# Kernel tuning notes

Hardware: AMD Instinct MI355X
Metric: run time of the kernel (lower is better)

## Reference

```python
import jax, jax.numpy as jnp
import numpy as np

EPS = 1e-5

def _ln(x, w, b):
    mu = jnp.mean(x, -1, keepdims=True)
    var = jnp.mean((x - mu) ** 2, -1, keepdims=True)
    return (x - mu) * jax.lax.rsqrt(var + EPS) * w + b

def setup_inputs() -> dict:
    key = jax.random.key(0)
    ks = jax.random.split(key, 12)
    B, H, W, C = 4, 32, 32, 768
    nh, hd, hidden = 12, 64, 3072
    s = lambda k, sh, fan: jax.random.normal(k, sh, jnp.float32) * (fan ** -0.5)
    return {
        "x": jax.random.normal(ks[0], (B, H, W, C), jnp.float32),
        "norm1_w": jnp.ones((C,), jnp.float32),
        "norm1_b": jnp.zeros((C,), jnp.float32),
        "qkv_w": s(ks[1], (C, 3 * C), C),
        "qkv_b": jnp.zeros((3 * C,), jnp.float32),
        "proj_w": s(ks[2], (C, C), C),
        "proj_b": jnp.zeros((C,), jnp.float32),
        "rel_h": jnp.ones((2 * H - 1, hd), jnp.float32),
        "rel_w": jnp.ones((2 * W - 1, hd), jnp.float32),
        "norm2_w": jnp.ones((C,), jnp.float32),
        "norm2_b": jnp.zeros((C,), jnp.float32),
        "mlp_w1": s(ks[3], (C, hidden), C),
        "mlp_b1": jnp.zeros((hidden,), jnp.float32),
        "mlp_w2": s(ks[4], (hidden, C), hidden),
        "mlp_b2": jnp.zeros((C,), jnp.float32),
    }

def reference(x, norm1_w, norm1_b, qkv_w, qkv_b, proj_w, proj_b, rel_h, rel_w,
              norm2_w, norm2_b, mlp_w1, mlp_b1, mlp_w2, mlp_b2):
    B, H, W, C = x.shape
    nh = 12
    hd = C // nh
    scale = hd ** -0.5
    S = H * W

    xn = _ln(x, norm1_w, norm1_b)
    qkv = (xn.reshape(B, S, C) @ qkv_w + qkv_b)            # [B,S,3C]
    qkv = qkv.reshape(B, S, 3, nh, hd).transpose(2, 0, 3, 1, 4).reshape(3, B * nh, S, hd)
    q, k, v = qkv[0], qkv[1], qkv[2]                        # [B*nh,S,hd]

    attn = jnp.einsum('bqd,bkd->bqk', q * scale, k)         # [B*nh,S,S]

    # relative position bias (q_size == k_size == H or W)
    idx_h = jnp.arange(H)[:, None] - jnp.arange(H)[None, :] + (H - 1)
    idx_w = jnp.arange(W)[:, None] - jnp.arange(W)[None, :] + (W - 1)
    Rh = rel_h[idx_h]                                       # [H,H,hd]
    Rw = rel_w[idx_w]                                       # [W,W,hd]
    q4 = q.reshape(B * nh, H, W, hd)                        # unscaled q, as in source
    bias_h = jnp.einsum('bhwc,hkc->bhwk', q4, Rh)           # [B*nh,H,W,H]
    bias_w = jnp.einsum('bhwc,wkc->bhwk', q4, Rw)           # [B*nh,H,W,W]
    attn = (attn.reshape(B * nh, H, W, H, W)
            + bias_h[:, :, :, :, None]
            + bias_w[:, :, :, None, :]).reshape(B * nh, S, S)

    attn = jax.nn.softmax(attn, axis=-1)
    out = jnp.einsum('bqk,bkd->bqd', attn, v)               # [B*nh,S,hd]
    out = out.reshape(B, nh, H, W, hd).transpose(0, 2, 3, 1, 4).reshape(B, H, W, C)
    x = out @ proj_w + proj_b + x

    xn = _ln(x, norm2_w, norm2_b)
    h = jax.nn.gelu(xn @ mlp_w1 + mlp_b1, approximate=False)
    return h @ mlp_w2 + mlp_b2 + x
```

## Files before the change

kernel.cpp:

```cpp
#include <hip/hip_runtime.h>
#include <hip/hip_bf16.h>
#include <cstdint>
#include <cstddef>

typedef __bf16 bf16x8 __attribute__((ext_vector_type(8)));
typedef float  f32x4  __attribute__((ext_vector_type(4)));
typedef unsigned short u16x8 __attribute__((ext_vector_type(8)));

#define S_TOT 1024
#define NH 12
#define HD 64
#define NBH 48
#define CDIM 768
#define L2E 1.44269504088896f

static __device__ __forceinline__ unsigned short f2bf(float f) {
    unsigned int u = __builtin_bit_cast(unsigned int, f);
    u += 0x7FFFu + ((u >> 16) & 1u);
    return (unsigned short)(u >> 16);
}

static __device__ __forceinline__ float exp2_raw(float x) {
    float r;
    asm("v_exp_f32 %0, %1" : "=v"(r) : "v"(x));
    return r;
}

static __device__ __forceinline__ float gelu_fast(float x) {
    float u = x * (1.0f + 0.044715f * x * x);
    float e = exp2_raw(-2.3022090f * u);
    return x / (1.0f + e);
}

static __device__ __forceinline__ void async16(void* lds, const void* g) {
    __builtin_amdgcn_global_load_lds(
        (const __attribute__((address_space(1))) unsigned int*)g,
        (__attribute__((address_space(3))) unsigned int*)lds, 16, 0, 0);
}

static __device__ __forceinline__ void xcd_part(int orig, int& bm_idx, int& bn_idx) {
    bm_idx = ((orig & 7) << 3) + ((orig >> 3) & 7);
    bn_idx = orig >> 6;
}

__launch_bounds__(256)
__global__ void ln_kernel(const float* __restrict__ x, const float* __restrict__ w,
                          const float* __restrict__ b, unsigned short* __restrict__ out)
{
    const int row = blockIdx.x;
    const int tid = threadIdx.x;
    const float* xr = x + (size_t)row * CDIM;
    float v0 = xr[tid], v1 = xr[tid + 256], v2 = xr[tid + 512];
    float s  = v0 + v1 + v2;
    float s2 = v0 * v0 + v1 * v1 + v2 * v2;
    #pragma unroll
    for (int off = 32; off > 0; off >>= 1) {
        s  += __shfl_xor(s,  off);
        s2 += __shfl_xor(s2, off);
    }
    __shared__ float ss[4], ss2[4];
    const int wid = tid >> 6;
    if ((tid & 63) == 0) { ss[wid] = s; ss2[wid] = s2; }
    __syncthreads();
    s  = ss[0] + ss[1] + ss[2] + ss[3];
    s2 = ss2[0] + ss2[1] + ss2[2] + ss2[3];
    const float mu  = s * (1.0f / CDIM);
    const float var = s2 * (1.0f / CDIM) - mu * mu;
    const float rs  = rsqrtf(var + 1e-5f);
    unsigned short* orow = out + (size_t)row * CDIM;
    float vv[3] = {v0, v1, v2};
    #pragma unroll
    for (int i = 0; i < 3; ++i) {
        int c = tid + i * 256;
        orow[c] = f2bf((vv[i] - mu) * rs * w[c] + b[c]);
    }
}

__launch_bounds__(256)
__global__ void wt_all_kernel(const float* __restrict__ qkv_w, const float* __restrict__ proj_w,
                              const float* __restrict__ w1, const float* __restrict__ w2,
                              unsigned short* __restrict__ wTq, unsigned short* __restrict__ wTp,
                              unsigned short* __restrict__ wT1, unsigned short* __restrict__ wT2)
{
    __shared__ float tile[32][33];
    int id = blockIdx.x;
    const float* W; unsigned short* WT; int K, N, ko, no;
    if (id < 1728)      { W = qkv_w;  WT = wTq; K = 768;  N = 2304;            ko = id % 24; no = id / 24; }
    else if (id < 2304) { W = proj_w; WT = wTp; K = 768;  N = 768;  id -= 1728; ko = id % 24; no = id / 24; }
    else if (id < 4608) { W = w1;     WT = wT1; K = 768;  N = 3072; id -= 2304; ko = id % 24; no = id / 24; }
    else                { W = w2;     WT = wT2; K = 3072; N = 768;  id -= 4608; ko = id % 96; no = id / 96; }
    const int k0 = ko * 32, n0 = no * 32;
    const int tx = threadIdx.x & 31, ty = threadIdx.x >> 5;
    #pragma unroll
    for (int i = 0; i < 4; ++i) {
        int kk = ty + i * 8;
        tile[kk][tx] = W[(size_t)(k0 + kk) * N + n0 + tx];
    }
    __syncthreads();
    #pragma unroll
    for (int i = 0; i < 4; ++i) {
        int nn = ty + i * 8;
        WT[(size_t)(n0 + nn) * K + k0 + tx] = f2bf(tile[tx][nn]);
    }
}

__launch_bounds__(256)
__global__ void vtrans_kernel(const unsigned short* __restrict__ v,
                              unsigned short* __restrict__ vT)
{
    __shared__ unsigned short tile[64][65];
    const int bh = blockIdx.x;
    const int s0 = blockIdx.y * 64;
    const int tid = threadIdx.x;
    #pragma unroll
    for (int it = 0; it < 2; ++it) {
        int idx = tid + it * 256;
        int r = idx >> 3, c0 = (idx & 7) * 8;
        *(u16x8*)&tile[r][c0] = *(const u16x8*)&v[((size_t)bh * S_TOT + s0 + r) * HD + c0];
    }
    __syncthreads();
    #pragma unroll
    for (int it = 0; it < 2; ++it) {
        int idx = tid + it * 256;
        int d = idx >> 3, sc = (idx & 7) * 8;
        u16x8 o;
        #pragma unroll
        for (int e = 0; e < 8; ++e) o[e] = tile[sc + e][d];
        *(u16x8*)&vT[((size_t)bh * HD + d) * S_TOT + s0 + sc] = o;
    }
}

template<int EPI>
__launch_bounds__(256)
__global__ void gemm64x128_kernel(const unsigned short* __restrict__ A,
                                  const unsigned short* __restrict__ BT,
                                  const float* __restrict__ bias,
                                  unsigned short* __restrict__ outh,
                                  int M, int N, int K)
{
    __shared__ __align__(16) unsigned short As[64 * 64];
    __shared__ __align__(16) unsigned short Bs[128 * 64];
    const int tid  = threadIdx.x;
    int bmi, bni;
    xcd_part(blockIdx.y * gridDim.x + blockIdx.x, bmi, bni);
    const int bm   = bmi * 64;
    const int bn   = bni * 128;
    const int wid  = tid >> 6, lane = tid & 63;
    const int wr   = (wid >> 1) * 32, wc = (wid & 1) * 64;
    const int fr   = lane & 15, fk = lane >> 4;

    f32x4 acc[2][4] = {};

    for (int kk = 0; kk < K; kk += 64) {
        __syncthreads();
        #pragma unroll
        for (int it = 0; it < 4; ++it) {
            int idx = tid + it * 256;
            int r = idx >> 3;
            int j = (idx & 7) ^ (r & 7);
            async16(&Bs[idx * 8], &BT[(size_t)(bn + r) * K + kk + j * 8]);
            if (it < 2)
                async16(&As[idx * 8], &A[(size_t)(bm + r) * K + kk + j * 8]);
        }
        __syncthreads();
        #pragma unroll
        for (int ks = 0; ks < 2; ++ks) {
            bf16x8 af[2], bfv[4];
            #pragma unroll
            for (int i = 0; i < 2; ++i) {
                int Ra = wr + i * 16 + fr;
                af[i] = *(const bf16x8*)&As[Ra * 64 + (((ks * 4 + fk) ^ (Ra & 7)) * 8)];
            }
            #pragma unroll
            for (int j = 0; j < 4; ++j) {
                int Rb = wc + j * 16 + fr;
                bfv[j] = *(const bf16x8*)&Bs[Rb * 64 + (((ks * 4 + fk) ^ (Rb & 7)) * 8)];
            }
            __builtin_amdgcn_s_setprio(1);
            #pragma unroll
            for (int i = 0; i < 2; ++i)
                #pragma unroll
                for (int j = 0; j < 4; ++j)
                    acc[i][j] = __builtin_amdgcn_mfma_f32_16x16x32_bf16(af[i], bfv[j], acc[i][j], 0, 0, 0);
            __builtin_amdgcn_s_setprio(0);
        }
    }

    const int er = (lane >> 4) * 4;
    const int ec = lane & 15;
    #pragma unroll
    for (int i = 0; i < 2; ++i) {
        const int rowb = bm + wr + i * 16 + er;
        #pragma unroll
        for (int j = 0; j < 4; ++j) {
            const int col = bn + wc + j * 16 + ec;
            #pragma unroll
            for (int r = 0; r < 4; ++r) {
                const int row = rowb + r;
                float val = acc[i][j][r] + bias[col];
                if constexpr (EPI == 0) {
                    int bb = row >> 10, s = row & 1023;
                    int t  = col / CDIM;
                    int rem = col - t * CDIM;
                    int hh = rem >> 6, d = rem & 63;
                    outh[((size_t)(t * NBH + bb * NH + hh) * S_TOT + s) * HD + d] = f2bf(val);
                } else {
                    outh[(size_t)row * N + col] = f2bf(gelu_fast(val));
                }
            }
        }
    }
}

__launch_bounds__(256)
__global__ void gemm64_kernel(const unsigned short* __restrict__ A,
                              const unsigned short* __restrict__ BT,
                              const float* __restrict__ bias,
                              const float* __restrict__ res,
                              float* __restrict__ outf,
                              int M, int N, int K)
{
    __shared__ __align__(16) unsigned short As[2][64 * 64];
    __shared__ __align__(16) unsigned short Bs[2][64 * 64];
    const int tid  = threadIdx.x;
    int bmi, bni;
    xcd_part(blockIdx.y * gridDim.x + blockIdx.x, bmi, bni);
    const int bm   = bmi * 64;
    const int bn   = bni * 64;
    const int wid  = tid >> 6, lane = tid & 63;
    const int wr   = (wid >> 1) * 32, wc = (wid & 1) * 32;
    const int fr   = lane & 15, fk = lane >> 4;

    f32x4 acc[2][2] = {};
    const int nt = K >> 6;

    #pragma unroll
    for (int it = 0; it < 2; ++it) {
        int idx = tid + it * 256;
        int r = idx >> 3;
        int j = (idx & 7) ^ (r & 7);
        async16(&As[0][idx * 8], &A[(size_t)(bm + r) * K + j * 8]);
        async16(&Bs[0][idx * 8], &BT[(size_t)(bn + r) * K + j * 8]);
    }

    int cur = 0;
    for (int t = 0; t < nt; ++t) {
        if (t + 1 < nt) {
            const int kk = (t + 1) << 6;
            #pragma unroll
            for (int it = 0; it < 2; ++it) {
                int idx = tid + it * 256;
                int r = idx >> 3;
                int j = (idx & 7) ^ (r & 7);
                async16(&As[cur ^ 1][idx * 8], &A[(size_t)(bm + r) * K + kk + j * 8]);
                async16(&Bs[cur ^ 1][idx * 8], &BT[(size_t)(bn + r) * K + kk + j * 8]);
            }
            asm volatile("s_waitcnt vmcnt(4)" ::: "memory");
        } else {
            asm volatile("s_waitcnt vmcnt(0)" ::: "memory");
        }
        __builtin_amdgcn_s_barrier();
        const unsigned short* Ac = As[cur];
        const unsigned short* Bc = Bs[cur];
        #pragma unroll
        for (int ks = 0; ks < 2; ++ks) {
            bf16x8 af[2], bfv[2];
            #pragma unroll
            for (int i = 0; i < 2; ++i) {
                int Ra = wr + i * 16 + fr;
                af[i]  = *(const bf16x8*)&Ac[Ra * 64 + (((ks * 4 + fk) ^ (Ra & 7)) * 8)];
                int Rb = wc + i * 16 + fr;
                bfv[i] = *(const bf16x8*)&Bc[Rb * 64 + (((ks * 4 + fk) ^ (Rb & 7)) * 8)];
            }
            __builtin_amdgcn_s_setprio(1);
            #pragma unroll
            for (int i = 0; i < 2; ++i)
                #pragma unroll
                for (int j = 0; j < 2; ++j)
                    acc[i][j] = __builtin_amdgcn_mfma_f32_16x16x32_bf16(af[i], bfv[j], acc[i][j], 0, 0, 0);
            __builtin_amdgcn_s_setprio(0);
        }
        __builtin_amdgcn_s_barrier();
        cur ^= 1;
    }

    const int er = (lane >> 4) * 4;
    const int ec = lane & 15;
    #pragma unroll
    for (int i = 0; i < 2; ++i) {
        const int rowb = bm + wr + i * 16 + er;
        #pragma unroll
        for (int j = 0; j < 2; ++j) {
            const int col = bn + wc + j * 16 + ec;
            #pragma unroll
            for (int r = 0; r < 4; ++r) {
                const int row = rowb + r;
                size_t idx = (size_t)row * N + col;
                outf[idx] = acc[i][j][r] + bias[col] + res[idx];
            }
        }
    }
}

__launch_bounds__(256)
__global__ void bias_kernel(const unsigned short* __restrict__ q,
                            const float* __restrict__ rel_h,
                            const float* __restrict__ rel_w,
                            float* __restrict__ biasH,
                            float* __restrict__ biasW)
{
    __shared__ __align__(16) unsigned short Bl[32 * 72];
    const int tid  = threadIdx.x;
    const int wid  = tid >> 6, lane = tid & 63;
    const int fr   = lane & 15, fk = lane >> 4;
    const int mt   = blockIdx.x;
    const int qc   = blockIdx.y;
    const int mode = blockIdx.z;
    const float* rel = mode ? rel_w : rel_h;
    float* outp = mode ? biasW : biasH;

    {
        int row = tid >> 3, c0 = (tid & 7) * 8;
        const float* rp = rel + (size_t)(qc + 31 - row) * HD + c0;
        u16x8 o;
        #pragma unroll
        for (int e = 0; e < 8; ++e) o[e] = f2bf(rp[e]);
        *(u16x8*)&Bl[row * 72 + c0] = o;
    }
    __syncthreads();

    const int ri = wid * 16 + fr;
    const int bh = mt * 2 + (ri >> 5);
    const int inner = ri & 31;
    const int s = mode ? (inner * 32 + qc) : (qc * 32 + inner);
    const unsigned short* arow = q + ((size_t)bh * S_TOT + s) * HD;

    f32x4 acc[2] = {};
    #pragma unroll
    for (int ks = 0; ks < 2; ++ks) {
        bf16x8 af = *(const bf16x8*)&arow[ks * 32 + fk * 8];
        #pragma unroll
        for (int nt = 0; nt < 2; ++nt) {
            bf16x8 bfv = *(const bf16x8*)&Bl[(nt * 16 + fr) * 72 + ks * 32 + fk * 8];
            acc[nt] = __builtin_amdgcn_mfma_f32_16x16x32_bf16(af, bfv, acc[nt], 0, 0, 0);
        }
    }

    const int g = lane >> 4, c = lane & 15;
    #pragma unroll
    for (int reg = 0; reg < 4; ++reg) {
        int ro = wid * 16 + g * 4 + reg;
        int bho = mt * 2 + (ro >> 5);
        int io  = ro & 31;
        int so  = mode ? (io * 32 + qc) : (qc * 32 + io);
        float* op = outp + ((size_t)bho * S_TOT + so) * 32;
        op[c]      = acc[0][reg] * L2E;
        op[16 + c] = acc[1][reg] * L2E;
    }
}

__launch_bounds__(256, 3)
__global__ void attn_kernel(const unsigned short* __restrict__ qkv,
                            const unsigned short* __restrict__ vT,
                            const float* __restrict__ biasH,
                            const float* __restrict__ biasW,
                            unsigned short* __restrict__ out)
{
    __shared__ __align__(16) unsigned short Ks[128 * 64];
    __shared__ __align__(16) unsigned short Vt[64 * 128];
    __shared__ __align__(16) unsigned short Pst[4][16][136];

    const int tid  = threadIdx.x;
    const int wid  = tid >> 6;
    const int lane = tid & 63;
    const int fr   = lane & 15, fk = lane >> 4;
    const int er   = (lane >> 4) * 4, ec = lane & 15;
    const int bh_  = blockIdx.x % NBH;
    const int qt   = blockIdx.x / NBH;
    const int row0 = qt * 64;
    const int b    = bh_ / NH, h = bh_ - b * NH;

    const unsigned short* q = qkv;
    const unsigned short* k = qkv + (size_t)NBH * S_TOT * HD;
    const size_t headoff  = (size_t)bh_ * S_TOT * HD;
    const size_t vheadoff = (size_t)bh_ * HD * S_TOT;

    #pragma unroll
    for (int it = 0; it < 2; ++it) {
        int idx = tid + it * 256;
        int r = idx >> 3;
        int j = (idx & 7) ^ (r & 7);
        async16(&Ks[idx * 8], &q[headoff + (size_t)(row0 + r) * HD + j * 8]);
    }
    __syncthreads();

    bf16x8 qf[2];
    {
        int Rq = wid * 16 + fr;
        qf[0] = *(const bf16x8*)&Ks[Rq * 64 + ((fk ^ (Rq & 7)) * 8)];
        qf[1] = *(const bf16x8*)&Ks[Rq * 64 + (((4 + fk) ^ (Rq & 7)) * 8)];
    }

    float bh0[4], bh1[4], bw0[4], bw1[4];
    {
        const int g = lane >> 4, c = lane & 15;
        #pragma unroll
        for (int reg = 0; reg < 4; ++reg) {
            int rt = row0 + wid * 16 + g * 4 + reg;
            const float* ph = biasH + ((size_t)bh_ * S_TOT + rt) * 32;
            const float* pw = biasW + ((size_t)bh_ * S_TOT + rt) * 32;
            bh0[reg] = ph[c];  bh1[reg] = ph[16 + c];
            bw0[reg] = pw[c];  bw1[reg] = pw[16 + c];
        }
    }

    const u16x8 ones_u = {0x3F80, 0x3F80, 0x3F80, 0x3F80, 0x3F80, 0x3F80, 0x3F80, 0x3F80};
    const bf16x8 ones = __builtin_bit_cast(bf16x8, ones_u);
    const float SCL = 0.125f * L2E;

    float m[4], l[4];
    f32x4 oacc[4];
    #pragma unroll
    for (int r = 0; r < 4; ++r) {
        m[r] = -1e30f; l[r] = 0.f;
        oacc[r][0] = 0.f; oacc[r][1] = 0.f; oacc[r][2] = 0.f; oacc[r][3] = 0.f;
    }

    for (int KT = 0; KT < 8; ++KT) {
        __syncthreads();
        #pragma unroll
        for (int it = 0; it < 4; ++it) {
            int idx = tid + it * 256;
            int r = idx >> 3;
            int j = (idx & 7) ^ (r & 7);
            async16(&Ks[idx * 8], &k[headoff + (size_t)(KT * 128 + r) * HD + j * 8]);
        }
        #pragma unroll
        for (int it = 0; it < 4; ++it) {
            int idx = tid + it * 256;
            int r = idx >> 4;
            int j = (idx & 15) ^ (r & 7);
            async16(&Vt[idx * 8], &vT[vheadoff + (size_t)r * S_TOT + KT * 128 + j * 8]);
        }
        __syncthreads();

        f32x4 sacc[8];
        #pragma unroll
        for (int nt = 0; nt < 8; ++nt) {
            sacc[nt][0] = 0.f; sacc[nt][1] = 0.f; sacc[nt][2] = 0.f; sacc[nt][3] = 0.f;
        }
        __builtin_amdgcn_s_setprio(1);
        #pragma unroll
        for (int nt = 0; nt < 8; ++nt) {
            int Rk = nt * 16 + fr;
            bf16x8 b0 = *(const bf16x8*)&Ks[Rk * 64 + ((fk ^ (Rk & 7)) * 8)];
            bf16x8 b1 = *(const bf16x8*)&Ks[Rk * 64 + (((4 + fk) ^ (Rk & 7)) * 8)];
            sacc[nt] = __builtin_amdgcn_mfma_f32_16x16x32_bf16(qf[0], b0, sacc[nt], 0, 0, 0);
            sacc[nt] = __builtin_amdgcn_mfma_f32_16x16x32_bf16(qf[1], b1, sacc[nt], 0, 0, 0);
        }
        __builtin_amdgcn_s_setprio(0);

        float bhv[4][4];
        #pragma unroll
        for (int jj = 0; jj < 4; ++jj) {
            int kh = KT * 4 + jj;
            int src = ((lane >> 4) << 4) + (kh & 15);
            #pragma unroll
            for (int reg = 0; reg < 4; ++reg)
                bhv[jj][reg] = (kh < 16) ? __shfl(bh0[reg], src) : __shfl(bh1[reg], src);
        }

        float tmax[4] = {-1e30f, -1e30f, -1e30f, -1e30f};
        #pragma unroll
        for (int nt = 0; nt < 8; ++nt) {
            #pragma unroll
            for (int reg = 0; reg < 4; ++reg) {
                float s_ = sacc[nt][reg] * SCL + bhv[nt >> 1][reg]
                         + ((nt & 1) ? bw1[reg] : bw0[reg]);
                sacc[nt][reg] = s_;
                tmax[reg] = fmaxf(tmax[reg], s_);
            }
        }
        #pragma unroll
        for (int reg = 0; reg < 4; ++reg) {
            #pragma unroll
            for (int off = 8; off > 0; off >>= 1)
                tmax[reg] = fmaxf(tmax[reg], __shfl_xor(tmax[reg], off));
            float mnew = fmaxf(m[reg], tmax[reg]);
            float c = exp2_raw(m[reg] - mnew);
            m[reg] = mnew;
            #pragma unroll
            for (int nt = 0; nt < 8; ++nt) {
                float p = exp2_raw(sacc[nt][reg] - mnew);
                Pst[wid][er + reg][nt * 16 + ec] = f2bf(p);
            }
            l[reg] *= c;
            #pragma unroll
            for (int nt = 0; nt < 4; ++nt) oacc[nt][reg] *= c;
        }

        __builtin_amdgcn_s_setprio(1);
        bf16x8 pa[4];
        #pragma unroll
        for (int ks = 0; ks < 4; ++ks)
            pa[ks] = *(const bf16x8*)&Pst[wid][fr][ks * 32 + fk * 8];
        f32x4 ps = {};
        #pragma unroll
        for (int ks = 0; ks < 4; ++ks)
            ps = __builtin_amdgcn_mfma_f32_16x16x32_bf16(pa[ks], ones, ps, 0, 0, 0);
        #pragma unroll
        for (int nt = 0; nt < 4; ++nt) {
            int Rv = nt * 16 + fr;
            #pragma unroll
            for (int ks = 0; ks < 4; ++ks) {
                int ch = (ks * 4 + fk) ^ (Rv & 7);
                bf16x8 vb = *(const bf16x8*)&Vt[Rv * 128 + ch * 8];
                oacc[nt] = __builtin_amdgcn_mfma_f32_16x16x32_bf16(pa[ks], vb, oacc[nt], 0, 0, 0);
            }
        }
        __builtin_amdgcn_s_setprio(0);
        #pragma unroll
        for (int reg = 0; reg < 4; ++reg) l[reg] += ps[reg];
    }

    #pragma unroll
    for (int reg = 0; reg < 4; ++reg) {
        float inv = 1.0f / l[reg];
        int srow = row0 + wid * 16 + er + reg;
        #pragma unroll
        for (int nt = 0; nt < 4; ++nt) {
            out[((size_t)(b * S_TOT + srow)) * CDIM + h * HD + nt * 16 + ec] =
                f2bf(oacc[nt][reg] * inv);
        }
    }
}

extern "C" void kernel_launch(void* const* d_in, const int* in_sizes, int n_in,
                              void* d_out, int out_size, void* d_ws, size_t ws_size,
                              hipStream_t stream)
{
    const float* x      = (const float*)d_in[0];
    const float* n1w    = (const float*)d_in[1];
    const float* n1b    = (const float*)d_in[2];
    const float* qkv_w  = (const float*)d_in[3];
    const float* qkv_b  = (const float*)d_in[4];
    const float* proj_w = (const float*)d_in[5];
    const float* proj_b = (const float*)d_in[6];
    const float* rel_h  = (const float*)d_in[7];
    const float* rel_w  = (const float*)d_in[8];
    const float* n2w    = (const float*)d_in[9];
    const float* n2b    = (const float*)d_in[10];
    const float* w1     = (const float*)d_in[11];
    const float* b1     = (const float*)d_in[12];
    const float* w2     = (const float*)d_in[13];
    const float* b2     = (const float*)d_in[14];

    char* ws = (char*)d_ws;
    unsigned short* qkvbf = (unsigned short*)(ws + 0);
    float*          biasH = (float*)(ws + 18874368);
    float*          biasW = (float*)(ws + 25165824);
    unsigned short* hbf   = (unsigned short*)(ws + 0);
    float*          x1    = (float*)(ws + 25165824);
    unsigned short* xnbf  = (unsigned short*)(ws + 37748736);
    unsigned short* vTbuf = (unsigned short*)(ws + 37748736);
    unsigned short* wTq   = (unsigned short*)(ws + 44040192);
    unsigned short* wTp   = (unsigned short*)(ws + 47579136);
    unsigned short* wT1   = (unsigned short*)(ws + 48758784);
    unsigned short* wT2   = (unsigned short*)(ws + 53477376);
    unsigned short* aout  = (unsigned short*)(ws + 58195968);

    wt_all_kernel<<<6912, 256, 0, stream>>>(qkv_w, proj_w, w1, w2, wTq, wTp, wT1, wT2);

    ln_kernel<<<4096, 256, 0, stream>>>(x, n1w, n1b, xnbf);
    gemm64x128_kernel<0><<<dim3(64, 18), 256, 0, stream>>>(xnbf, wTq, qkv_b, qkvbf, 4096, 2304, 768);
    vtrans_kernel<<<dim3(48, 16), 256, 0, stream>>>(qkvbf + (size_t)2 * NBH * S_TOT * HD, vTbuf);
    bias_kernel<<<dim3(24, 32, 2), 256, 0, stream>>>(qkvbf, rel_h, rel_w, biasH, biasW);
    attn_kernel<<<768, 256, 0, stream>>>(qkvbf, vTbuf, biasH, biasW, aout);
    gemm64_kernel<<<dim3(64, 12), 256, 0, stream>>>(aout, wTp, proj_b, x, x1, 4096, 768, 768);
    ln_kernel<<<4096, 256, 0, stream>>>(x1, n2w, n2b, xnbf);
    gemm64x128_kernel<2><<<dim3(64, 24), 256, 0, stream>>>(xnbf, wT1, b1, hbf, 4096, 3072, 768);
    gemm64_kernel<<<dim3(64, 12), 256, 0, stream>>>(hbf, wT2, b2, x1, (float*)d_out, 4096, 768, 3072);
}
```

Baseline: 174.9 us.

## Widen GEMM K-tile to 128 and drop double buffering in gemm64

Both GEMM kernels now stage 128-wide K slices in shared memory instead of 64, halving the number of barrier/load rounds per tile. The gemm64 kernel loses its double-buffered prefetch pipeline and becomes a simple load-sync-compute loop with the larger tile. This trades fewer synchronisations for lost overlap of global loads with MFMA work, and doubles LDS use per block, which may reduce occupancy.

```diff
diff --git a/kernel.cpp b/kernel.cpp
--- a/kernel.cpp
+++ b/kernel.cpp
@@ -138,8 +138,8 @@
                                   unsigned short* __restrict__ outh,
                                   int M, int N, int K)
 {
-    __shared__ __align__(16) unsigned short As[64 * 64];
-    __shared__ __align__(16) unsigned short Bs[128 * 64];
+    __shared__ __align__(16) unsigned short As[64 * 128];
+    __shared__ __align__(16) unsigned short Bs[128 * 128];
     const int tid  = threadIdx.x;
     int bmi, bni;
     xcd_part(blockIdx.y * gridDim.x + blockIdx.x, bmi, bni);
@@ -151,30 +151,30 @@
 
     f32x4 acc[2][4] = {};
 
-    for (int kk = 0; kk < K; kk += 64) {
+    for (int kk = 0; kk < K; kk += 128) {
         __syncthreads();
         #pragma unroll
-        for (int it = 0; it < 4; ++it) {
+        for (int it = 0; it < 8; ++it) {
             int idx = tid + it * 256;
-            int r = idx >> 3;
-            int j = (idx & 7) ^ (r & 7);
-            async16(&Bs[idx * 8], &BT[(size_t)(bn + r) * K + kk + j * 8]);
-            if (it < 2)
-                async16(&As[idx * 8], &A[(size_t)(bm + r) * K + kk + j * 8]);
+            int r = idx >> 4;
+            int jj = (idx & 15) ^ (r & 7);
+            async16(&Bs[idx * 8], &BT[(size_t)(bn + r) * K + kk + jj * 8]);
+            if (it < 4)
+                async16(&As[idx * 8], &A[(size_t)(bm + r) * K + kk + jj * 8]);
         }
         __syncthreads();
         #pragma unroll
-        for (int ks = 0; ks < 2; ++ks) {
+        for (int ks = 0; ks < 4; ++ks) {
             bf16x8 af[2], bfv[4];
             #pragma unroll
             for (int i = 0; i < 2; ++i) {
                 int Ra = wr + i * 16 + fr;
-                af[i] = *(const bf16x8*)&As[Ra * 64 + (((ks * 4 + fk) ^ (Ra & 7)) * 8)];
+                af[i] = *(const bf16x8*)&As[Ra * 128 + (((ks * 4 + fk) ^ (Ra & 7)) * 8)];
             }
             #pragma unroll
             for (int j = 0; j < 4; ++j) {
                 int Rb = wc + j * 16 + fr;
-                bfv[j] = *(const bf16x8*)&Bs[Rb * 64 + (((ks * 4 + fk) ^ (Rb & 7)) * 8)];
+                bfv[j] = *(const bf16x8*)&Bs[Rb * 128 + (((ks * 4 + fk) ^ (Rb & 7)) * 8)];
             }
             __builtin_amdgcn_s_setprio(1);
             #pragma unroll
@@ -220,8 +220,8 @@
                               float* __restrict__ outf,
                               int M, int N, int K)
 {
-    __shared__ __align__(16) unsigned short As[2][64 * 64];
-    __shared__ __align__(16) unsigned short Bs[2][64 * 64];
+    __shared__ __align__(16) unsigned short As[64 * 128];
+    __shared__ __align__(16) unsigned short Bs[64 * 128];
     const int tid  = threadIdx.x;
     int bmi, bni;
     xcd_part(blockIdx.y * gridDim.x + blockIdx.x, bmi, bni);
@@ -232,45 +232,27 @@
     const int fr   = lane & 15, fk = lane >> 4;
 
     f32x4 acc[2][2] = {};
-    const int nt = K >> 6;
-
-    #pragma unroll
-    for (int it = 0; it < 2; ++it) {
-        int idx = tid + it * 256;
-        int r = idx >> 3;
-        int j = (idx & 7) ^ (r & 7);
-        async16(&As[0][idx * 8], &A[(size_t)(bm + r) * K + j * 8]);
-        async16(&Bs[0][idx * 8], &BT[(size_t)(bn + r) * K + j * 8]);
-    }
-
-    int cur = 0;
-    for (int t = 0; t < nt; ++t) {
-        if (t + 1 < nt) {
-            const int kk = (t + 1) << 6;
-            #pragma unroll
-            for (int it = 0; it < 2; ++it) {
-                int idx = tid + it * 256;
-                int r = idx >> 3;
-                int j = (idx & 7) ^ (r & 7);
-                async16(&As[cur ^ 1][idx * 8], &A[(size_t)(bm + r) * K + kk + j * 8]);
-                async16(&Bs[cur ^ 1][idx * 8], &BT[(size_t)(bn + r) * K + kk + j * 8]);
-            }
-            asm volatile("s_waitcnt vmcnt(4)" ::: "memory");
-        } else {
-            asm volatile("s_waitcnt vmcnt(0)" ::: "memory");
-        }
-        __builtin_amdgcn_s_barrier();
-        const unsigned short* Ac = As[cur];
-        const unsigned short* Bc = Bs[cur];
-        #pragma unroll
-        for (int ks = 0; ks < 2; ++ks) {
+
+    for (int kk = 0; kk < K; kk += 128) {
+        __syncthreads();
+        #pragma unroll
+        for (int it = 0; it < 4; ++it) {
+            int idx = tid + it * 256;
+            int r = idx >> 4;
+            int jj = (idx & 15) ^ (r & 7);
+            async16(&As[idx * 8], &A[(size_t)(bm + r) * K + kk + jj * 8]);
+            async16(&Bs[idx * 8], &BT[(size_t)(bn + r) * K + kk + jj * 8]);
+        }
+        __syncthreads();
+        #pragma unroll
+        for (int ks = 0; ks < 4; ++ks) {
             bf16x8 af[2], bfv[2];
             #pragma unroll
             for (int i = 0; i < 2; ++i) {
                 int Ra = wr + i * 16 + fr;
-                af[i]  = *(const bf16x8*)&Ac[Ra * 64 + (((ks * 4 + fk) ^ (Ra & 7)) * 8)];
+                af[i]  = *(const bf16x8*)&As[Ra * 128 + (((ks * 4 + fk) ^ (Ra & 7)) * 8)];
                 int Rb = wc + i * 16 + fr;
-                bfv[i] = *(const bf16x8*)&Bc[Rb * 64 + (((ks * 4 + fk) ^ (Rb & 7)) * 8)];
+                bfv[i] = *(const bf16x8*)&Bs[Rb * 128 + (((ks * 4 + fk) ^ (Rb & 7)) * 8)];
             }
             __builtin_amdgcn_s_setprio(1);
             #pragma unroll
@@ -280,8 +262,6 @@
                     acc[i][j] = __builtin_amdgcn_mfma_f32_16x16x32_bf16(af[i], bfv[j], acc[i][j], 0, 0, 0);
             __builtin_amdgcn_s_setprio(0);
         }
-        __builtin_amdgcn_s_barrier();
-        cur ^= 1;
     }
 
     const int er = (lane >> 4) * 4;
```

New measurement: 164.0 us. 1.07x faster.
